# Optimization experiments

Hardware: AMD Instinct MI355X
Metric: run time of the kernel (lower is better)

Reference implementation:

```python
import jax, jax.numpy as jnp
import numpy as np

B = 64
RX, RZ, RX_, RZ_ = 32, 16, 16, 8
TN = 1
STRIDE = 2
IN_DIM, OUT_DIM = 256, 512
KEY_DIM, H, ATTN_RATIO = 32, 8, 2
D = ATTN_RATIO * KEY_DIM            # per-head value dim = 64
DH = D * H                          # 512
NH_KD = KEY_DIM * H                 # 256
N = RX * RX + TN * RZ * RZ          # 1280 tokens (search + template)
N_ = RX_ * RX_ + TN * RZ_ * RZ_     # 320 subsampled query tokens
SCALE = KEY_DIM ** -0.5
EPS = 1e-5


def linear_bn(x, W, gamma, beta):
    # Linear (no bias) followed by BatchNorm1d in training mode over (B*N, C)
    y = jnp.einsum('bnc,oc->bno', x, W)
    m = y.mean(axis=(0, 1))
    v = y.var(axis=(0, 1))  # biased variance, as torch BN uses for normalization
    return (y - m) * jax.lax.rsqrt(v + EPS) * gamma + beta


def subsample(x):
    # stride-subsample the search-region tokens and each template's tokens
    b, n, c = x.shape
    parts = [x[:, :RX * RX].reshape(b, RX, RX, c)[:, ::STRIDE, ::STRIDE].reshape(b, -1, c)]
    for i in range(TN):
        s = RX * RX + i * RZ * RZ
        z = x[:, s:s + RZ * RZ].reshape(b, RZ, RZ, c)[:, ::STRIDE, ::STRIDE].reshape(b, -1, c)
        parts.append(z)
    return jnp.concatenate(parts, axis=1)


def setup_inputs() -> dict:
    key = jax.random.key(0)
    ks = jax.random.split(key, 4)
    return {
        'x': jax.random.normal(ks[0], (B, N, IN_DIM), dtype=jnp.float32),
        'W_kv': jax.random.normal(ks[1], (NH_KD + DH, IN_DIM), dtype=jnp.float32) * 0.02,
        'g_kv': jnp.ones((NH_KD + DH,), jnp.float32),
        'b_kv': jnp.zeros((NH_KD + DH,), jnp.float32),
        'W_q': jax.random.normal(ks[2], (NH_KD, IN_DIM), dtype=jnp.float32) * 0.02,
        'g_q': jnp.ones((NH_KD,), jnp.float32),
        'b_q': jnp.zeros((NH_KD,), jnp.float32),
        'W_p': jax.random.normal(ks[3], (OUT_DIM, DH), dtype=jnp.float32) * 0.02,
        'g_p': jnp.ones((OUT_DIM,), jnp.float32),
        'b_p': jnp.zeros((OUT_DIM,), jnp.float32),
    }


def reference(x, W_kv, g_kv, b_kv, W_q, g_q, b_q, W_p, g_p, b_p):
    b = x.shape[0]
    # fused KV projection + BN, then split into per-head K and V
    kv = linear_bn(x, W_kv, g_kv, b_kv).reshape(b, N, H, KEY_DIM + D)
    k = kv[..., :KEY_DIM].transpose(0, 2, 1, 3)   # [B,H,N,key_dim]
    v = kv[..., KEY_DIM:].transpose(0, 2, 1, 3)   # [B,H,N,d]
    # Q: subsample tokens, then Linear_BN
    q = linear_bn(subsample(x), W_q, g_q, b_q).reshape(b, N_, H, KEY_DIM).transpose(0, 2, 1, 3)
    attn = jax.nn.softmax(jnp.einsum('bhqd,bhkd->bhqk', q, k) * SCALE, axis=-1)
    o = jnp.einsum('bhqk,bhkd->bhqd', attn, v).transpose(0, 2, 1, 3).reshape(b, N_, DH)
    return linear_bn(jax.nn.hard_swish(o), W_p, g_p, b_p)
```

## Files before the change

### kernel.cpp

```cpp
#include <hip/hip_runtime.h>
#include <hip/hip_bf16.h>
#include <math.h>

#define EPSF 1e-5f
#define SCALEF 0.17677669529663687f

typedef unsigned short u16;
typedef unsigned int u32;
typedef __attribute__((ext_vector_type(8))) short bf16x8;
typedef __attribute__((ext_vector_type(4))) float f32x4;

__device__ __forceinline__ float b2f(u16 u) {
    union { unsigned int i; float f; } v; v.i = ((unsigned int)u) << 16; return v.f;
}
__device__ __forceinline__ u16 f2b(float f) {
    union { float f; unsigned int i; } v; v.f = f;
    unsigned int x = v.i;
    return (u16)((x + 0x7fffu + ((x >> 16) & 1u)) >> 16);
}

__global__ void convert_f32_bf16(const float* __restrict__ src, u16* __restrict__ dst, int n4) {
    int i = blockIdx.x * 256 + threadIdx.x;
    if (i >= n4) return;
    float4 v = ((const float4*)src)[i];
    ushort4 o;
    o.x = f2b(v.x); o.y = f2b(v.y); o.z = f2b(v.z); o.w = f2b(v.w);
    ((ushort4*)dst)[i] = o;
}

__global__ void gather_sub_bf16(const u16* __restrict__ xb, u16* __restrict__ xsub, int n8) {
    int i = blockIdx.x * 256 + threadIdx.x;
    if (i >= n8) return;
    int e = i << 3;
    int row = e >> 8;
    int col = e & 255;
    int b = row / 320;
    int t = row - b * 320;
    int n;
    if (t < 256) n = ((t >> 4) << 6) + ((t & 15) << 1);
    else { int tt = t - 256; n = 1024 + ((tt >> 3) << 5) + ((tt & 7) << 1); }
    *(int4*)(xsub + e) = *(const int4*)(xb + ((size_t)(b * 1280 + n)) * 256 + col);
}

template<int OUT_F32>
__global__ __launch_bounds__(256) void gemm_bt(const u16* __restrict__ A, const u16* __restrict__ Bw,
                                               void* __restrict__ Cv, int M, int N, int K,
                                               float* __restrict__ sums) {
    __shared__ u16 As[128 * 40];
    __shared__ u16 Bs[128 * 40];
    __shared__ float sumbuf[4][64][2];
    const int tid = threadIdx.x;
    const int wave = tid >> 6, lane = tid & 63;
    const int quad = lane >> 4, lc = lane & 15;
    const int wr = wave >> 1, wc = wave & 1;
    const int m0 = blockIdx.x * 128, n0 = blockIdx.y * 128;
    const int lrow = tid >> 2;
    const int lk = (tid & 3) << 3;

    f32x4 acc[4][4];
#pragma unroll
    for (int i = 0; i < 4; ++i)
#pragma unroll
        for (int j = 0; j < 4; ++j) acc[i][j] = (f32x4){0.f, 0.f, 0.f, 0.f};

    for (int k0 = 0; k0 < K; k0 += 32) {
        __syncthreads();
        *(int4*)&As[lrow * 40 + lk]        = *(const int4*)(A  + (size_t)(m0 + lrow) * K + k0 + lk);
        *(int4*)&As[(lrow + 64) * 40 + lk] = *(const int4*)(A  + (size_t)(m0 + lrow + 64) * K + k0 + lk);
        *(int4*)&Bs[lrow * 40 + lk]        = *(const int4*)(Bw + (size_t)(n0 + lrow) * K + k0 + lk);
        *(int4*)&Bs[(lrow + 64) * 40 + lk] = *(const int4*)(Bw + (size_t)(n0 + lrow + 64) * K + k0 + lk);
        __syncthreads();
        bf16x8 af[4], bfr[4];
#pragma unroll
        for (int mi = 0; mi < 4; ++mi) af[mi]  = *(const bf16x8*)&As[(wr * 64 + mi * 16 + lc) * 40 + quad * 8];
#pragma unroll
        for (int ni = 0; ni < 4; ++ni) bfr[ni] = *(const bf16x8*)&Bs[(wc * 64 + ni * 16 + lc) * 40 + quad * 8];
#pragma unroll
        for (int mi = 0; mi < 4; ++mi)
#pragma unroll
            for (int ni = 0; ni < 4; ++ni)
                acc[mi][ni] = __builtin_amdgcn_mfma_f32_16x16x32_bf16(af[mi], bfr[ni], acc[mi][ni], 0, 0, 0);
    }
    float ps[4], ps2[4];
#pragma unroll
    for (int ni = 0; ni < 4; ++ni) { ps[ni] = 0.f; ps2[ni] = 0.f; }
#pragma unroll
    for (int mi = 0; mi < 4; ++mi)
#pragma unroll
        for (int ni = 0; ni < 4; ++ni)
#pragma unroll
            for (int r = 0; r < 4; ++r) {
                int row = m0 + wr * 64 + mi * 16 + quad * 4 + r;
                int cn  = n0 + wc * 64 + ni * 16 + lc;
                float v = acc[mi][ni][r];
                ps[ni] += v; ps2[ni] += v * v;
                if (OUT_F32) ((float*)Cv)[(size_t)row * N + cn] = v;
                else         ((u16*)Cv)[(size_t)row * N + cn] = f2b(v);
            }
#pragma unroll
    for (int ni = 0; ni < 4; ++ni) {
        ps[ni]  += __shfl_xor(ps[ni], 16);  ps[ni]  += __shfl_xor(ps[ni], 32);
        ps2[ni] += __shfl_xor(ps2[ni], 16); ps2[ni] += __shfl_xor(ps2[ni], 32);
    }
    if (quad == 0) {
#pragma unroll
        for (int ni = 0; ni < 4; ++ni) {
            sumbuf[wave][ni * 16 + lc][0] = ps[ni];
            sumbuf[wave][ni * 16 + lc][1] = ps2[ni];
        }
    }
    __syncthreads();
    {
        int which = tid & 1, idx = (tid >> 1) & 63, wcg = tid >> 7;
        int channel = n0 + wcg * 64 + idx;
        float v = sumbuf[wcg][idx][which] + sumbuf[wcg + 2][idx][which];
        int rep = blockIdx.x & 7;
        atomicAdd(&sums[(rep * 2 + which) * N + channel], v);
    }
}

__global__ void finalize_bn(const float* __restrict__ sum2, const float* __restrict__ g,
                            const float* __restrict__ beta, int cols, float inv_n, float scale,
                            float* __restrict__ AB) {
    int c = blockIdx.x * 256 + threadIdx.x;
    if (c >= cols) return;
    float s = 0.f, s2 = 0.f;
#pragma unroll
    for (int r = 0; r < 8; ++r) {
        s  += sum2[(r * 2 + 0) * cols + c];
        s2 += sum2[(r * 2 + 1) * cols + c];
    }
    float m = s * inv_n;
    float var = s2 * inv_n - m * m;
    float a = g[c] * rsqrtf(var + EPSF) * scale;
    AB[c] = a;
    AB[cols + c] = beta[c] * scale - m * a;
}

__global__ __launch_bounds__(256) void normalize_kv(const u16* __restrict__ kv, const float* __restrict__ AB,
                                                    u16* __restrict__ Kn, u16* __restrict__ Vtn) {
    __shared__ u16 Vs[64 * 66];
    const int h = blockIdx.x, nt = blockIdx.y, b = blockIdx.z;
    const int bh = b * 8 + h;
    const int tid = threadIdx.x;
    {
        int tok = tid >> 2, dk = (tid & 3) << 3;
        size_t src = ((size_t)(b * 1280 + nt * 64 + tok)) * 768 + h * 96 + dk;
        union { int4 v; u16 u[8]; } ld; ld.v = *(const int4*)(kv + src);
        union { int4 v; u16 u[8]; } st;
#pragma unroll
        for (int j = 0; j < 8; ++j) {
            int c = h * 96 + dk + j;
            st.u[j] = f2b(b2f(ld.u[j]) * AB[c] + AB[768 + c]);
        }
        int g = tok >> 5, kk = tok & 31;
        int rowp = nt * 64 + g * 32 + ((kk & 1) << 4) + (kk >> 1);
        *(int4*)(Kn + ((size_t)bh * 1280 + rowp) * 32 + dk) = st.v;
    }
#pragma unroll
    for (int half = 0; half < 2; ++half) {
        int t = (tid >> 3) + half * 32;
        int dv = (tid & 7) << 3;
        size_t src = ((size_t)(b * 1280 + nt * 64 + t)) * 768 + h * 96 + 32 + dv;
        union { int4 v; u16 u[8]; } ld; ld.v = *(const int4*)(kv + src);
#pragma unroll
        for (int j = 0; j < 8; ++j) {
            int c = h * 96 + 32 + dv + j;
            Vs[(dv + j) * 66 + t] = f2b(b2f(ld.u[j]) * AB[c] + AB[768 + c]);
        }
    }
    __syncthreads();
#pragma unroll
    for (int half = 0; half < 2; ++half) {
        int d = (tid >> 3) + half * 32;
        int tc = (tid & 7) << 3;
        union { int4 v; u16 u[8]; } st;
#pragma unroll
        for (int j = 0; j < 8; ++j) st.u[j] = Vs[d * 66 + tc + j];
        *(int4*)(Vtn + ((size_t)bh * 64 + d) * 1280 + nt * 64 + tc) = st.v;
    }
}

__global__ __launch_bounds__(256, 2) void attn_kernel3(const u16* __restrict__ Kn, const u16* __restrict__ Vtn,
                                                       const u16* __restrict__ q_raw, const float* __restrict__ ABq,
                                                       u16* __restrict__ o_act) {
    __shared__ u16 Ps[4 * 5 * 640];
    const int tid = threadIdx.x;
    const int wave = tid >> 6, lane = tid & 63;
    const int quad = lane >> 4, lc = lane & 15;
    const int h = blockIdx.x, b = blockIdx.y;
    const int bh = b * 8 + h;

    float qa[8], qb[8];
#pragma unroll
    for (int j = 0; j < 8; ++j) { int c = h * 32 + quad * 8 + j; qa[j] = ABq[c]; qb[j] = ABq[256 + c]; }
    bf16x8 qf[5];
#pragma unroll
    for (int j = 0; j < 5; ++j) {
        const u16* qs = q_raw + ((size_t)(b * 320 + j * 64 + wave * 16 + lc)) * 256 + h * 32 + quad * 8;
        union { int4 v; u16 u[8]; } ld; ld.v = *(const int4*)qs;
        union { bf16x8 v; u16 u[8]; } st;
#pragma unroll
        for (int jj = 0; jj < 8; ++jj) st.u[jj] = f2b(b2f(ld.u[jj]) * qa[jj] + qb[jj]);
        qf[j] = st.v;
    }

    const u16* Kp = Kn + (size_t)bh * 1280 * 32 + lc * 32 + quad * 8;
    const u16* Vp = Vtn + (size_t)bh * 64 * 1280 + lc * 1280 + quad * 8;
    u16* Pw = &Ps[wave * 5 * 640];

    f32x4 acc[5][4];
#pragma unroll
    for (int j = 0; j < 5; ++j)
#pragma unroll
        for (int i = 0; i < 4; ++i) acc[j][i] = (f32x4){0.f, 0.f, 0.f, 0.f};
    float lsum[5][4];
#pragma unroll
    for (int j = 0; j < 5; ++j)
#pragma unroll
        for (int r = 0; r < 4; ++r) lsum[j][r] = 0.f;

    for (int kc = 0; kc < 1280; kc += 32) {
        bf16x8 kf0 = *(const bf16x8*)(Kp + kc * 32);
        bf16x8 kf1 = *(const bf16x8*)(Kp + kc * 32 + 512);
        bf16x8 vf0 = *(const bf16x8*)(Vp + kc);
        bf16x8 vf1 = *(const bf16x8*)(Vp + 16 * 1280 + kc);
        bf16x8 vf2 = *(const bf16x8*)(Vp + 32 * 1280 + kc);
        bf16x8 vf3 = *(const bf16x8*)(Vp + 48 * 1280 + kc);
        f32x4 z = (f32x4){0.f, 0.f, 0.f, 0.f};
        f32x4 s0[5], s1[5];
#pragma unroll
        for (int j = 0; j < 5; ++j) {
            s0[j] = __builtin_amdgcn_mfma_f32_16x16x32_bf16(qf[j], kf0, z, 0, 0, 0);
            s1[j] = __builtin_amdgcn_mfma_f32_16x16x32_bf16(qf[j], kf1, z, 0, 0, 0);
        }
#pragma unroll
        for (int j = 0; j < 5; ++j)
#pragma unroll
            for (int r = 0; r < 4; ++r) {
                float p0 = __expf(s0[j][r]);
                float p1 = __expf(s1[j][r]);
                lsum[j][r] += p0 + p1;
                u32 pk = (u32)f2b(p0) | ((u32)f2b(p1) << 16);
                *(u32*)&Pw[j * 640 + (quad * 4 + r) * 40 + 2 * lc] = pk;
            }
#pragma unroll
        for (int j = 0; j < 5; ++j) {
            bf16x8 pf = *(const bf16x8*)&Pw[j * 640 + lc * 40 + quad * 8];
            acc[j][0] = __builtin_amdgcn_mfma_f32_16x16x32_bf16(pf, vf0, acc[j][0], 0, 0, 0);
            acc[j][1] = __builtin_amdgcn_mfma_f32_16x16x32_bf16(pf, vf1, acc[j][1], 0, 0, 0);
            acc[j][2] = __builtin_amdgcn_mfma_f32_16x16x32_bf16(pf, vf2, acc[j][2], 0, 0, 0);
            acc[j][3] = __builtin_amdgcn_mfma_f32_16x16x32_bf16(pf, vf3, acc[j][3], 0, 0, 0);
        }
    }
#pragma unroll
    for (int j = 0; j < 5; ++j) {
        float inv[4];
#pragma unroll
        for (int r = 0; r < 4; ++r) {
            float l = lsum[j][r];
            l += __shfl_xor(l, 1);
            l += __shfl_xor(l, 2);
            l += __shfl_xor(l, 4);
            l += __shfl_xor(l, 8);
            inv[r] = 1.f / l;
        }
        int qrow = b * 320 + j * 64 + wave * 16 + quad * 4;
#pragma unroll
        for (int nt = 0; nt < 4; ++nt)
#pragma unroll
            for (int r = 0; r < 4; ++r) {
                float o = acc[j][nt][r] * inv[r];
                float hs = o * fminf(fmaxf(o + 3.f, 0.f), 6.f) * (1.f / 6.f);
                o_act[(size_t)(qrow + r) * 512 + h * 64 + nt * 16 + lc] = f2b(hs);
            }
    }
}

__global__ void bn_apply_out(const float* __restrict__ praw, const float* __restrict__ ABp,
                             float* __restrict__ out, int n4) {
    int i = blockIdx.x * 256 + threadIdx.x;
    if (i >= n4) return;
    int e = i << 2;
    int c = e & 511;
    float4 v = ((const float4*)praw)[i];
    float4 o;
    o.x = v.x * ABp[c]     + ABp[512 + c];
    o.y = v.y * ABp[c + 1] + ABp[512 + c + 1];
    o.z = v.z * ABp[c + 2] + ABp[512 + c + 2];
    o.w = v.w * ABp[c + 3] + ABp[512 + c + 3];
    ((float4*)out)[i] = o;
}

extern "C" void kernel_launch(void* const* d_in, const int* in_sizes, int n_in,
                              void* d_out, int out_size, void* d_ws, size_t ws_size,
                              hipStream_t stream) {
    const float* x   = (const float*)d_in[0];
    const float* Wkv = (const float*)d_in[1];
    const float* gkv = (const float*)d_in[2];
    const float* bkv = (const float*)d_in[3];
    const float* Wq  = (const float*)d_in[4];
    const float* gq  = (const float*)d_in[5];
    const float* bq  = (const float*)d_in[6];
    const float* Wp  = (const float*)d_in[7];
    const float* gp  = (const float*)d_in[8];
    const float* bp  = (const float*)d_in[9];
    float* out = (float*)d_out;

    char* ws = (char*)d_ws;
    size_t off = 0;
    auto alloc = [&](size_t bytes) -> void* {
        void* p = ws + off;
        off += (bytes + 255) & ~(size_t)255;
        return p;
    };
    u16*   kv_raw = (u16*)alloc(81920ull * 768 * 2);
    u16*   q_raw  = (u16*)alloc(20480ull * 256 * 2);
    void*  slot1  = alloc(81920ull * 256 * 2);
    u16*   x_b    = (u16*)slot1;
    u16*   K_norm = (u16*)slot1;
    float* p_raw  = (float*)slot1;
    void*  slot2  = alloc(20480ull * 512 * 2);
    u16*   xsub_b = (u16*)slot2;
    u16*   o_act  = (u16*)slot2;
    u16*   Vt_norm = (u16*)alloc(512ull * 64 * 1280 * 2);
    u16*   Wkv_b  = (u16*)alloc(768ull * 256 * 2);
    u16*   Wq_b   = (u16*)alloc(256ull * 256 * 2);
    u16*   Wp_b   = (u16*)alloc(512ull * 512 * 2);
    float* sums_kv = (float*)alloc(8 * 2 * 768 * sizeof(float));
    float* sums_q  = (float*)alloc(8 * 2 * 256 * sizeof(float));
    float* sums_p  = (float*)alloc(8 * 2 * 512 * sizeof(float));
    float* ABkv = (float*)alloc(1536 * sizeof(float));
    float* ABq  = (float*)alloc(512 * sizeof(float));
    float* ABp  = (float*)alloc(1024 * sizeof(float));

    dim3 blk(256);
    hipMemsetAsync(sums_kv, 0, 8 * 2 * (768 + 256 + 512) * sizeof(float), stream);

    convert_f32_bf16<<<20480, blk, 0, stream>>>(x,   x_b,   5242880);
    convert_f32_bf16<<<192,   blk, 0, stream>>>(Wkv, Wkv_b, 49152);
    convert_f32_bf16<<<64,    blk, 0, stream>>>(Wq,  Wq_b,  16384);
    convert_f32_bf16<<<256,   blk, 0, stream>>>(Wp,  Wp_b,  65536);
    gather_sub_bf16<<<2560,   blk, 0, stream>>>(x_b, xsub_b, 655360);

    gemm_bt<0><<<dim3(640, 6), blk, 0, stream>>>(x_b, Wkv_b, kv_raw, 81920, 768, 256, sums_kv);
    gemm_bt<0><<<dim3(160, 2), blk, 0, stream>>>(xsub_b, Wq_b, q_raw, 20480, 256, 256, sums_q);

    finalize_bn<<<3, blk, 0, stream>>>(sums_kv, gkv, bkv, 768, 1.f / 81920.f, 1.f, ABkv);
    finalize_bn<<<1, blk, 0, stream>>>(sums_q,  gq,  bq,  256, 1.f / 20480.f, SCALEF, ABq);

    normalize_kv<<<dim3(8, 20, 64), blk, 0, stream>>>(kv_raw, ABkv, K_norm, Vt_norm);

    attn_kernel3<<<dim3(8, 64), blk, 0, stream>>>(K_norm, Vt_norm, q_raw, ABq, o_act);

    gemm_bt<1><<<dim3(160, 4), blk, 0, stream>>>(o_act, Wp_b, p_raw, 20480, 512, 512, sums_p);
    finalize_bn<<<2, blk, 0, stream>>>(sums_p, gp, bp, 512, 1.f / 20480.f, 1.f, ABp);

    bn_apply_out<<<10240, blk, 0, stream>>>(p_raw, ABp, out, 2621440);
}
```

Baseline: 426.2 us.

## Compute KV batchnorm stats from Gram matrix and fuse normalization into KV GEMM

Derives the KV BatchNorm mean and variance from column sums and the input Gram matrix X^T X combined with W. This lets the KV GEMM epilogue apply normalization directly and write K and transposed V, removing the bf16 kv_raw round trip and the separate normalize kernel. The attention kernel double-buffers P through LDS so the PV MFMAs overlap the next chunk's QK and exp. It also computes the row sums with an MFMA against a ones vector, uses exp2 with log2e folded into the Q scale, and truncates instead of rounding when packing P. The Gram path adds extra kernels and a 16MB partial buffer, and it computes variance as E[y^2]-m^2, which carries some numerical risk.

```diff
diff --git a/kernel.cpp b/kernel.cpp
--- a/kernel.cpp
+++ b/kernel.cpp
@@ -4,6 +4,7 @@
 
 #define EPSF 1e-5f
 #define SCALEF 0.17677669529663687f
+#define LOG2E 1.4426950408889634f
 
 typedef unsigned short u16;
 typedef unsigned int u32;
@@ -17,6 +18,23 @@
     union { float f; unsigned int i; } v; v.f = f;
     unsigned int x = v.i;
     return (u16)((x + 0x7fffu + ((x >> 16) & 1u)) >> 16);
+}
+__device__ __forceinline__ u32 fbits(float f) {
+    union { float f; u32 u; } v; v.f = f; return v.u;
+}
+__device__ __forceinline__ float dexp2(float x) {
+#if __has_builtin(__builtin_amdgcn_exp2f)
+    return __builtin_amdgcn_exp2f(x);
+#else
+    return exp2f(x);
+#endif
+}
+__device__ __forceinline__ u32 pack_trunc(float p0, float p1) {
+#if __has_builtin(__builtin_amdgcn_perm)
+    return __builtin_amdgcn_perm(fbits(p1), fbits(p0), 0x07060302u);
+#else
+    return (fbits(p0) >> 16) | (fbits(p1) & 0xffff0000u);
+#endif
 }
 
 __global__ void convert_f32_bf16(const float* __restrict__ src, u16* __restrict__ dst, int n4) {
@@ -40,6 +58,112 @@
     if (t < 256) n = ((t >> 4) << 6) + ((t & 15) << 1);
     else { int tt = t - 256; n = 1024 + ((tt >> 3) << 5) + ((tt & 7) << 1); }
     *(int4*)(xsub + e) = *(const int4*)(xb + ((size_t)(b * 1280 + n)) * 256 + col);
+}
+
+__global__ void colsum256(const u16* __restrict__ X, int rowsPerBlock, float* __restrict__ out) {
+    int c = threadIdx.x;
+    int r0 = blockIdx.x * rowsPerBlock;
+    float s = 0.f;
+    for (int r = 0; r < rowsPerBlock; ++r) s += b2f(X[(size_t)(r0 + r) * 256 + c]);
+    atomicAdd(&out[c], s);
+}
+
+__global__ __launch_bounds__(512) void gram256(const u16* __restrict__ X, int rowsPerBlock,
+                                               float* __restrict__ Gpart) {
+    __shared__ u16 Tt[256 * 72];
+    const int tid = threadIdx.x;
+    const int rp = tid & 31, cg = tid >> 5;
+    const int wv = tid >> 6, lane = tid & 63;
+    const int quad = lane >> 4, lc = lane & 15;
+    const int wm = wv >> 1, wn = wv & 1;
+    const int r0 = blockIdx.x * rowsPerBlock;
+
+    f32x4 acc[4][8];
+#pragma unroll
+    for (int i = 0; i < 4; ++i)
+#pragma unroll
+        for (int j = 0; j < 8; ++j) acc[i][j] = (f32x4){0.f, 0.f, 0.f, 0.f};
+
+    for (int rc = 0; rc < rowsPerBlock; rc += 64) {
+        __syncthreads();
+        union { int4 v; u16 u[8]; } ld[2][2];
+        size_t base = (size_t)(r0 + rc + rp * 2) * 256 + cg * 16;
+        ld[0][0].v = *(const int4*)(X + base);
+        ld[0][1].v = *(const int4*)(X + base + 8);
+        ld[1][0].v = *(const int4*)(X + base + 256);
+        ld[1][1].v = *(const int4*)(X + base + 264);
+        u32* T32 = (u32*)Tt;
+#pragma unroll
+        for (int j = 0; j < 16; ++j) {
+            u32 pk = (u32)ld[0][j >> 3].u[j & 7] | ((u32)ld[1][j >> 3].u[j & 7] << 16);
+            T32[(cg * 16 + j) * 36 + rp] = pk;
+        }
+        __syncthreads();
+#pragma unroll
+        for (int k0 = 0; k0 < 64; k0 += 32) {
+            bf16x8 af[4], bfr[8];
+#pragma unroll
+            for (int mi = 0; mi < 4; ++mi) af[mi] = *(const bf16x8*)&Tt[(wm * 64 + mi * 16 + lc) * 72 + k0 + quad * 8];
+#pragma unroll
+            for (int ni = 0; ni < 8; ++ni) bfr[ni] = *(const bf16x8*)&Tt[(wn * 128 + ni * 16 + lc) * 72 + k0 + quad * 8];
+#pragma unroll
+            for (int mi = 0; mi < 4; ++mi)
+#pragma unroll
+                for (int ni = 0; ni < 8; ++ni)
+                    acc[mi][ni] = __builtin_amdgcn_mfma_f32_16x16x32_bf16(af[mi], bfr[ni], acc[mi][ni], 0, 0, 0);
+        }
+    }
+    float* out = Gpart + (size_t)blockIdx.x * 65536;
+#pragma unroll
+    for (int mi = 0; mi < 4; ++mi)
+#pragma unroll
+        for (int ni = 0; ni < 8; ++ni)
+#pragma unroll
+            for (int r = 0; r < 4; ++r)
+                out[(wm * 64 + mi * 16 + quad * 4 + r) * 256 + wn * 128 + ni * 16 + lc] = acc[mi][ni][r];
+}
+
+__global__ void reduce_gpart(const float* __restrict__ Gp, float* __restrict__ G, int nz) {
+    int i = blockIdx.x * 256 + threadIdx.x;
+    float4 s = {0.f, 0.f, 0.f, 0.f};
+    for (int z = 0; z < nz; ++z) {
+        float4 v = ((const float4*)(Gp + (size_t)z * 65536))[i];
+        s.x += v.x; s.y += v.y; s.z += v.z; s.w += v.w;
+    }
+    ((float4*)G)[i] = s;
+}
+
+__global__ void stats_from_gram(const float* __restrict__ G, const float* __restrict__ colsum,
+                                const u16* __restrict__ Wb, const float* __restrict__ g,
+                                const float* __restrict__ beta, float inv_n, float scale,
+                                int cols, float* __restrict__ AB) {
+    const int c = blockIdx.x, t = threadIdx.x;
+    __shared__ float wsh[256];
+    __shared__ float red[4][2];
+    wsh[t] = b2f(Wb[c * 256 + t]);
+    __syncthreads();
+    float wt = wsh[t];
+    float acc = 0.f;
+#pragma unroll 4
+    for (int j = 0; j < 256; ++j) acc += G[j * 256 + t] * wsh[j];
+    float vterm = wt * acc;
+    float mterm = wt * colsum[t];
+#pragma unroll
+    for (int d = 1; d < 64; d <<= 1) {
+        vterm += __shfl_xor(vterm, d);
+        mterm += __shfl_xor(mterm, d);
+    }
+    if ((t & 63) == 0) { red[t >> 6][0] = vterm; red[t >> 6][1] = mterm; }
+    __syncthreads();
+    if (t == 0) {
+        float V = red[0][0] + red[1][0] + red[2][0] + red[3][0];
+        float M = red[0][1] + red[1][1] + red[2][1] + red[3][1];
+        float m = M * inv_n;
+        float var = V * inv_n - m * m;
+        float a = g[c] * rsqrtf(var + EPSF) * scale;
+        AB[c] = a;
+        AB[cols + c] = beta[c] * scale - m * a;
+    }
 }
 
 template<int OUT_F32>
@@ -137,54 +261,85 @@
     AB[cols + c] = beta[c] * scale - m * a;
 }
 
-__global__ __launch_bounds__(256) void normalize_kv(const u16* __restrict__ kv, const float* __restrict__ AB,
-                                                    u16* __restrict__ Kn, u16* __restrict__ Vtn) {
-    __shared__ u16 Vs[64 * 66];
-    const int h = blockIdx.x, nt = blockIdx.y, b = blockIdx.z;
-    const int bh = b * 8 + h;
+__global__ __launch_bounds__(256) void gemm_kv_fused(const u16* __restrict__ A, const u16* __restrict__ Bw,
+                                                     const float* __restrict__ AB,
+                                                     u16* __restrict__ Kn, u16* __restrict__ Vtn) {
+    __shared__ u16 As[128 * 40];
+    __shared__ u16 Bs[128 * 40];
+    __shared__ u16 Tws[4 * 1152];
     const int tid = threadIdx.x;
-    {
-        int tok = tid >> 2, dk = (tid & 3) << 3;
-        size_t src = ((size_t)(b * 1280 + nt * 64 + tok)) * 768 + h * 96 + dk;
-        union { int4 v; u16 u[8]; } ld; ld.v = *(const int4*)(kv + src);
-        union { int4 v; u16 u[8]; } st;
-#pragma unroll
-        for (int j = 0; j < 8; ++j) {
-            int c = h * 96 + dk + j;
-            st.u[j] = f2b(b2f(ld.u[j]) * AB[c] + AB[768 + c]);
-        }
-        int g = tok >> 5, kk = tok & 31;
-        int rowp = nt * 64 + g * 32 + ((kk & 1) << 4) + (kk >> 1);
-        *(int4*)(Kn + ((size_t)bh * 1280 + rowp) * 32 + dk) = st.v;
-    }
-#pragma unroll
-    for (int half = 0; half < 2; ++half) {
-        int t = (tid >> 3) + half * 32;
-        int dv = (tid & 7) << 3;
-        size_t src = ((size_t)(b * 1280 + nt * 64 + t)) * 768 + h * 96 + 32 + dv;
-        union { int4 v; u16 u[8]; } ld; ld.v = *(const int4*)(kv + src);
-#pragma unroll
-        for (int j = 0; j < 8; ++j) {
-            int c = h * 96 + 32 + dv + j;
-            Vs[(dv + j) * 66 + t] = f2b(b2f(ld.u[j]) * AB[c] + AB[768 + c]);
-        }
-    }
-    __syncthreads();
-#pragma unroll
-    for (int half = 0; half < 2; ++half) {
-        int d = (tid >> 3) + half * 32;
-        int tc = (tid & 7) << 3;
-        union { int4 v; u16 u[8]; } st;
-#pragma unroll
-        for (int j = 0; j < 8; ++j) st.u[j] = Vs[d * 66 + tc + j];
-        *(int4*)(Vtn + ((size_t)bh * 64 + d) * 1280 + nt * 64 + tc) = st.v;
-    }
-}
-
-__global__ __launch_bounds__(256, 2) void attn_kernel3(const u16* __restrict__ Kn, const u16* __restrict__ Vtn,
+    const int wave = tid >> 6, lane = tid & 63;
+    const int quad = lane >> 4, lc = lane & 15;
+    const int wr = wave >> 1, wc = wave & 1;
+    const int m0 = blockIdx.x * 128, n0 = blockIdx.y * 128;
+    const int lrow = tid >> 2;
+    const int lk = (tid & 3) << 3;
+    const int K = 256;
+
+    f32x4 acc[4][4];
+#pragma unroll
+    for (int i = 0; i < 4; ++i)
+#pragma unroll
+        for (int j = 0; j < 4; ++j) acc[i][j] = (f32x4){0.f, 0.f, 0.f, 0.f};
+
+    for (int k0 = 0; k0 < K; k0 += 32) {
+        __syncthreads();
+        *(int4*)&As[lrow * 40 + lk]        = *(const int4*)(A  + (size_t)(m0 + lrow) * K + k0 + lk);
+        *(int4*)&As[(lrow + 64) * 40 + lk] = *(const int4*)(A  + (size_t)(m0 + lrow + 64) * K + k0 + lk);
+        *(int4*)&Bs[lrow * 40 + lk]        = *(const int4*)(Bw + (size_t)(n0 + lrow) * K + k0 + lk);
+        *(int4*)&Bs[(lrow + 64) * 40 + lk] = *(const int4*)(Bw + (size_t)(n0 + lrow + 64) * K + k0 + lk);
+        __syncthreads();
+        bf16x8 af[4], bfr[4];
+#pragma unroll
+        for (int mi = 0; mi < 4; ++mi) af[mi]  = *(const bf16x8*)&As[(wr * 64 + mi * 16 + lc) * 40 + quad * 8];
+#pragma unroll
+        for (int ni = 0; ni < 4; ++ni) bfr[ni] = *(const bf16x8*)&Bs[(wc * 64 + ni * 16 + lc) * 40 + quad * 8];
+#pragma unroll
+        for (int mi = 0; mi < 4; ++mi)
+#pragma unroll
+            for (int ni = 0; ni < 4; ++ni)
+                acc[mi][ni] = __builtin_amdgcn_mfma_f32_16x16x32_bf16(af[mi], bfr[ni], acc[mi][ni], 0, 0, 0);
+    }
+    const int bb_ = m0 / 1280;
+    const int tokbase = m0 - bb_ * 1280;
+    u16* Tw = &Tws[wave * 1152];
+#pragma unroll
+    for (int ni = 0; ni < 4; ++ni) {
+        int cg0 = n0 + wc * 64 + ni * 16;
+        int h = cg0 / 96;
+        int rem = cg0 - h * 96;
+        int c = cg0 + lc;
+        float aa = AB[c], bb2 = AB[768 + c];
+        if (rem < 32) {
+#pragma unroll
+            for (int mi = 0; mi < 4; ++mi)
+#pragma unroll
+                for (int r = 0; r < 4; ++r) {
+                    int n = tokbase + wr * 64 + mi * 16 + quad * 4 + r;
+                    int rowp = (n & ~31) | ((n & 1) << 4) | ((n & 31) >> 1);
+                    Kn[(((size_t)(bb_ * 8 + h)) * 1280 + rowp) * 32 + rem + lc] = f2b(acc[mi][ni][r] * aa + bb2);
+                }
+        } else {
+#pragma unroll
+            for (int mi = 0; mi < 4; ++mi)
+#pragma unroll
+                for (int r = 0; r < 4; ++r)
+                    Tw[lc * 72 + mi * 16 + quad * 4 + r] = f2b(acc[mi][ni][r] * aa + bb2);
+            int dvl = lane >> 2, tg = lane & 3;
+            int dv = rem - 32 + dvl;
+            size_t vbase = ((size_t)(bb_ * 8 + h) * 64 + dv) * 1280 + tokbase + wr * 64;
+            bf16x8 v0 = *(const bf16x8*)&Tw[dvl * 72 + tg * 8];
+            bf16x8 v1 = *(const bf16x8*)&Tw[dvl * 72 + 32 + tg * 8];
+            *(bf16x8*)(Vtn + vbase + tg * 8) = v0;
+            *(bf16x8*)(Vtn + vbase + 32 + tg * 8) = v1;
+        }
+    }
+}
+
+__global__ __launch_bounds__(256, 2) void attn_kernel4(const u16* __restrict__ Kn, const u16* __restrict__ Vtn,
                                                        const u16* __restrict__ q_raw, const float* __restrict__ ABq,
                                                        u16* __restrict__ o_act) {
-    __shared__ u16 Ps[4 * 5 * 640];
+    __shared__ u16 Ps[25600];
     const int tid = threadIdx.x;
     const int wave = tid >> 6, lane = tid & 63;
     const int quad = lane >> 4, lc = lane & 15;
@@ -206,65 +361,76 @@
     }
 
     const u16* Kp = Kn + (size_t)bh * 1280 * 32 + lc * 32 + quad * 8;
-    const u16* Vp = Vtn + (size_t)bh * 64 * 1280 + lc * 1280 + quad * 8;
-    u16* Pw = &Ps[wave * 5 * 640];
+    const u16* Vp = Vtn + ((size_t)bh * 64 + lc) * 1280 + quad * 8;
+    u16* Pw = &Ps[wave * 6400];
 
     f32x4 acc[5][4];
-#pragma unroll
-    for (int j = 0; j < 5; ++j)
+    f32x4 accl[5];
+#pragma unroll
+    for (int j = 0; j < 5; ++j) {
+        accl[j] = (f32x4){0.f, 0.f, 0.f, 0.f};
 #pragma unroll
         for (int i = 0; i < 4; ++i) acc[j][i] = (f32x4){0.f, 0.f, 0.f, 0.f};
-    float lsum[5][4];
-#pragma unroll
-    for (int j = 0; j < 5; ++j)
-#pragma unroll
-        for (int r = 0; r < 4; ++r) lsum[j][r] = 0.f;
+    }
+    bf16x8 ones;
+    { union { bf16x8 v; u16 u[8]; } o_;
+#pragma unroll
+      for (int i = 0; i < 8; ++i) o_.u[i] = 0x3F80;
+      ones = o_.v; }
+    bf16x8 vprev[4];
 
     for (int kc = 0; kc < 1280; kc += 32) {
+        const int buf = (kc >> 5) & 1;
         bf16x8 kf0 = *(const bf16x8*)(Kp + kc * 32);
         bf16x8 kf1 = *(const bf16x8*)(Kp + kc * 32 + 512);
         bf16x8 vf0 = *(const bf16x8*)(Vp + kc);
         bf16x8 vf1 = *(const bf16x8*)(Vp + 16 * 1280 + kc);
         bf16x8 vf2 = *(const bf16x8*)(Vp + 32 * 1280 + kc);
         bf16x8 vf3 = *(const bf16x8*)(Vp + 48 * 1280 + kc);
-        f32x4 z = (f32x4){0.f, 0.f, 0.f, 0.f};
-        f32x4 s0[5], s1[5];
+        if (kc) {
+            const u16* Pr = Pw + (buf ^ 1) * 3200;
+#pragma unroll
+            for (int j = 0; j < 5; ++j) {
+                bf16x8 pf = *(const bf16x8*)&Pr[j * 640 + lc * 40 + quad * 8];
+                acc[j][0] = __builtin_amdgcn_mfma_f32_16x16x32_bf16(pf, vprev[0], acc[j][0], 0, 0, 0);
+                acc[j][1] = __builtin_amdgcn_mfma_f32_16x16x32_bf16(pf, vprev[1], acc[j][1], 0, 0, 0);
+                acc[j][2] = __builtin_amdgcn_mfma_f32_16x16x32_bf16(pf, vprev[2], acc[j][2], 0, 0, 0);
+                acc[j][3] = __builtin_amdgcn_mfma_f32_16x16x32_bf16(pf, vprev[3], acc[j][3], 0, 0, 0);
+                accl[j]   = __builtin_amdgcn_mfma_f32_16x16x32_bf16(pf, ones,     accl[j],   0, 0, 0);
+            }
+        }
+        u16* Pb = Pw + buf * 3200;
 #pragma unroll
         for (int j = 0; j < 5; ++j) {
-            s0[j] = __builtin_amdgcn_mfma_f32_16x16x32_bf16(qf[j], kf0, z, 0, 0, 0);
-            s1[j] = __builtin_amdgcn_mfma_f32_16x16x32_bf16(qf[j], kf1, z, 0, 0, 0);
-        }
-#pragma unroll
-        for (int j = 0; j < 5; ++j)
+            f32x4 z = (f32x4){0.f, 0.f, 0.f, 0.f};
+            f32x4 s0 = __builtin_amdgcn_mfma_f32_16x16x32_bf16(qf[j], kf0, z, 0, 0, 0);
+            f32x4 s1 = __builtin_amdgcn_mfma_f32_16x16x32_bf16(qf[j], kf1, z, 0, 0, 0);
 #pragma unroll
             for (int r = 0; r < 4; ++r) {
-                float p0 = __expf(s0[j][r]);
-                float p1 = __expf(s1[j][r]);
-                lsum[j][r] += p0 + p1;
-                u32 pk = (u32)f2b(p0) | ((u32)f2b(p1) << 16);
-                *(u32*)&Pw[j * 640 + (quad * 4 + r) * 40 + 2 * lc] = pk;
+                float p0 = dexp2(s0[r]);
+                float p1 = dexp2(s1[r]);
+                *(u32*)&Pb[j * 640 + (quad * 4 + r) * 40 + 2 * lc] = pack_trunc(p0, p1);
             }
+        }
+        vprev[0] = vf0; vprev[1] = vf1; vprev[2] = vf2; vprev[3] = vf3;
+    }
+    {
+        const u16* Pr = Pw + 3200;
 #pragma unroll
         for (int j = 0; j < 5; ++j) {
-            bf16x8 pf = *(const bf16x8*)&Pw[j * 640 + lc * 40 + quad * 8];
-            acc[j][0] = __builtin_amdgcn_mfma_f32_16x16x32_bf16(pf, vf0, acc[j][0], 0, 0, 0);
-            acc[j][1] = __builtin_amdgcn_mfma_f32_16x16x32_bf16(pf, vf1, acc[j][1], 0, 0, 0);
-            acc[j][2] = __builtin_amdgcn_mfma_f32_16x16x32_bf16(pf, vf2, acc[j][2], 0, 0, 0);
-            acc[j][3] = __builtin_amdgcn_mfma_f32_16x16x32_bf16(pf, vf3, acc[j][3], 0, 0, 0);
+            bf16x8 pf = *(const bf16x8*)&Pr[j * 640 + lc * 40 + quad * 8];
+            acc[j][0] = __builtin_amdgcn_mfma_f32_16x16x32_bf16(pf, vprev[0], acc[j][0], 0, 0, 0);
+            acc[j][1] = __builtin_amdgcn_mfma_f32_16x16x32_bf16(pf, vprev[1], acc[j][1], 0, 0, 0);
+            acc[j][2] = __builtin_amdgcn_mfma_f32_16x16x32_bf16(pf, vprev[2], acc[j][2], 0, 0, 0);
+            acc[j][3] = __builtin_amdgcn_mfma_f32_16x16x32_bf16(pf, vprev[3], acc[j][3], 0, 0, 0);
+            accl[j]   = __builtin_amdgcn_mfma_f32_16x16x32_bf16(pf, ones,     accl[j],   0, 0, 0);
         }
     }
 #pragma unroll
     for (int j = 0; j < 5; ++j) {
         float inv[4];
 #pragma unroll
-        for (int r = 0; r < 4; ++r) {
-            float l = lsum[j][r];
-            l += __shfl_xor(l, 1);
-            l += __shfl_xor(l, 2);
-            l += __shfl_xor(l, 4);
-            l += __shfl_xor(l, 8);
-            inv[r] = 1.f / l;
-        }
+        for (int r = 0; r < 4; ++r) inv[r] = 1.f / accl[j][r];
         int qrow = b * 320 + j * 64 + wave * 16 + quad * 4;
 #pragma unroll
         for (int nt = 0; nt < 4; ++nt)
@@ -314,28 +480,30 @@
         off += (bytes + 255) & ~(size_t)255;
         return p;
     };
-    u16*   kv_raw = (u16*)alloc(81920ull * 768 * 2);
     u16*   q_raw  = (u16*)alloc(20480ull * 256 * 2);
     void*  slot1  = alloc(81920ull * 256 * 2);
     u16*   x_b    = (u16*)slot1;
-    u16*   K_norm = (u16*)slot1;
     float* p_raw  = (float*)slot1;
     void*  slot2  = alloc(20480ull * 512 * 2);
     u16*   xsub_b = (u16*)slot2;
     u16*   o_act  = (u16*)slot2;
-    u16*   Vt_norm = (u16*)alloc(512ull * 64 * 1280 * 2);
+    u16*   K_nat  = (u16*)alloc(64ull * 8 * 1280 * 32 * 2);
+    u16*   Vt     = (u16*)alloc(512ull * 64 * 1280 * 2);
     u16*   Wkv_b  = (u16*)alloc(768ull * 256 * 2);
     u16*   Wq_b   = (u16*)alloc(256ull * 256 * 2);
     u16*   Wp_b   = (u16*)alloc(512ull * 512 * 2);
-    float* sums_kv = (float*)alloc(8 * 2 * 768 * sizeof(float));
-    float* sums_q  = (float*)alloc(8 * 2 * 256 * sizeof(float));
-    float* sums_p  = (float*)alloc(8 * 2 * 512 * sizeof(float));
-    float* ABkv = (float*)alloc(1536 * sizeof(float));
-    float* ABq  = (float*)alloc(512 * sizeof(float));
-    float* ABp  = (float*)alloc(1024 * sizeof(float));
+    float* Gpart  = (float*)alloc(64ull * 65536 * 4);
+    float* G      = (float*)alloc(65536 * 4);
+    float* statz  = (float*)alloc((256 + 4096 + 8192) * 4);
+    float* colsum_x = statz;
+    float* sums_q   = statz + 256;
+    float* sums_p   = statz + 256 + 4096;
+    float* ABkv = (float*)alloc(1536 * 4);
+    float* ABq  = (float*)alloc(512 * 4);
+    float* ABp  = (float*)alloc(1024 * 4);
 
     dim3 blk(256);
-    hipMemsetAsync(sums_kv, 0, 8 * 2 * (768 + 256 + 512) * sizeof(float), stream);
+    hipMemsetAsync(statz, 0, (256 + 4096 + 8192) * 4, stream);
 
     convert_f32_bf16<<<20480, blk, 0, stream>>>(x,   x_b,   5242880);
     convert_f32_bf16<<<192,   blk, 0, stream>>>(Wkv, Wkv_b, 49152);
@@ -343,15 +511,18 @@
     convert_f32_bf16<<<256,   blk, 0, stream>>>(Wp,  Wp_b,  65536);
     gather_sub_bf16<<<2560,   blk, 0, stream>>>(x_b, xsub_b, 655360);
 
-    gemm_bt<0><<<dim3(640, 6), blk, 0, stream>>>(x_b, Wkv_b, kv_raw, 81920, 768, 256, sums_kv);
+    colsum256<<<256, blk, 0, stream>>>(x_b, 320, colsum_x);
+    gram256<<<64, dim3(512), 0, stream>>>(x_b, 1280, Gpart);
+    reduce_gpart<<<64, blk, 0, stream>>>(Gpart, G, 64);
+    stats_from_gram<<<768, blk, 0, stream>>>(G, colsum_x, Wkv_b, gkv, bkv,
+                                             1.f / 81920.f, 1.f, 768, ABkv);
+
     gemm_bt<0><<<dim3(160, 2), blk, 0, stream>>>(xsub_b, Wq_b, q_raw, 20480, 256, 256, sums_q);
-
-    finalize_bn<<<3, blk, 0, stream>>>(sums_kv, gkv, bkv, 768, 1.f / 81920.f, 1.f, ABkv);
-    finalize_bn<<<1, blk, 0, stream>>>(sums_q,  gq,  bq,  256, 1.f / 20480.f, SCALEF, ABq);
-
-    normalize_kv<<<dim3(8, 20, 64), blk, 0, stream>>>(kv_raw, ABkv, K_norm, Vt_norm);
-
-    attn_kernel3<<<dim3(8, 64), blk, 0, stream>>>(K_norm, Vt_norm, q_raw, ABq, o_act);
+    finalize_bn<<<1, blk, 0, stream>>>(sums_q, gq, bq, 256, 1.f / 20480.f, SCALEF * LOG2E, ABq);
+
+    gemm_kv_fused<<<dim3(640, 6), blk, 0, stream>>>(x_b, Wkv_b, ABkv, K_nat, Vt);
+
+    attn_kernel4<<<dim3(8, 64), blk, 0, stream>>>(K_nat, Vt, q_raw, ABq, o_act);
 
     gemm_bt<1><<<dim3(160, 4), blk, 0, stream>>>(o_act, Wp_b, p_raw, 20480, 512, 512, sums_p);
     finalize_bn<<<2, blk, 0, stream>>>(sums_p, gp, bp, 512, 1.f / 20480.f, 1.f, ABp);
```

Result: slower. 502.4 us (+17.9%).
